# Kernel optimization log

Hardware: AMD Instinct MI355X
Metric: run time of the kernel (lower is better)

## Reference

```python
import jax, jax.numpy as jnp
import numpy as np

N_NODES = 100000
N_EDGES = 1600000
D_FEAT = 64


def setup_inputs() -> dict:
    key = jax.random.key(0)
    k1, k2, k3, k4 = jax.random.split(key, 4)
    row = jnp.sort(jax.random.randint(k1, (N_EDGES,), 0, N_NODES, dtype=jnp.int32))
    col = jax.random.randint(k2, (N_EDGES,), 0, N_NODES, dtype=jnp.int32)
    values = jax.random.uniform(k3, (N_EDGES,), dtype=jnp.float32)
    x = jax.random.normal(k4, (N_NODES, D_FEAT), dtype=jnp.float32)
    return {"row": row, "col": col, "values": values, "x": x}


def reference(row, col, values, x):
    # spmm_scatter: out[row[e]] += values[e] * x[col[e]]  (gather-multiply-scatter)
    msgs = x[col] * values[:, None]                      # [E, d]
    out = jax.ops.segment_sum(msgs, row, num_segments=x.shape[0])  # [N, d]
    return out
```

## Files before the change

kernel.cpp:

```cpp
#include <hip/hip_runtime.h>


constexpr int D  = 64;
constexpr int DV = D / 4;

__global__ __launch_bounds__(256) void spmm_psearch(
    const int* __restrict__ row,
    const int* __restrict__ col,
    const float* __restrict__ val,
    const float4* __restrict__ x4,
    float4* __restrict__ out4,
    int nEdges, int nNodes)
{
    const int wid = (blockIdx.x * blockDim.x + threadIdx.x) >> 6;
    if (wid >= nNodes) return;
    const int lane  = threadIdx.x & 63;
    const int group = lane >> 4;
    const int sub   = lane & 15;

    int lo = 0, hi = nEdges;
    const int t0 = wid;
    while (hi > lo) {
        const int span = hi - lo + 1;
        if (span <= 64) {
            const int idx = lo + lane;
            const bool lt = (idx <= hi) && (idx < nEdges) && (row[idx] < t0);
            lo += __popcll(__ballot(lt));
            break;
        }
        const int step = (span + 63) >> 6;
        const int idx  = lo + lane * step;
        const bool lt  = (idx <= hi) && (idx < nEdges) && (row[idx] < t0);
        const int  c   = __popcll(__ballot(lt));
        if (c == 0) { hi = lo; break; }
        const int new_lo = lo + (c - 1) * step + 1;
        if (c < 64) hi = lo + c * step;
        lo = new_lo;
    }
    const int start = lo;

    const int t1 = wid + 1;
    int end = start;
    for (;;) {
        const int idx = end + lane;
        const bool lt = (idx < nEdges) && (row[idx] < t1);
        const int  c  = __popcll(__ballot(lt));
        end += c;
        if (c < 64) break;
    }

    float4 acc = {0.f, 0.f, 0.f, 0.f};
    for (int e = start + group; e < end; e += 16) {
        const int e1 = e + 4, e2 = e + 8, e3 = e + 12;
        const int   c0 = col[e];
        const float v0 = val[e];
        int c1 = c0, c2 = c0, c3 = c0;
        float v1 = 0.f, v2 = 0.f, v3 = 0.f;
        if (e1 < end) { c1 = col[e1]; v1 = val[e1]; }
        if (e2 < end) { c2 = col[e2]; v2 = val[e2]; }
        if (e3 < end) { c3 = col[e3]; v3 = val[e3]; }
        const float4 x0 = x4[(size_t)c0 * DV + sub];
        const float4 x1 = x4[(size_t)c1 * DV + sub];
        const float4 x2 = x4[(size_t)c2 * DV + sub];
        const float4 x3 = x4[(size_t)c3 * DV + sub];
        acc.x = fmaf(v0, x0.x, acc.x); acc.y = fmaf(v0, x0.y, acc.y);
        acc.z = fmaf(v0, x0.z, acc.z); acc.w = fmaf(v0, x0.w, acc.w);
        acc.x = fmaf(v1, x1.x, acc.x); acc.y = fmaf(v1, x1.y, acc.y);
        acc.z = fmaf(v1, x1.z, acc.z); acc.w = fmaf(v1, x1.w, acc.w);
        acc.x = fmaf(v2, x2.x, acc.x); acc.y = fmaf(v2, x2.y, acc.y);
        acc.z = fmaf(v2, x2.z, acc.z); acc.w = fmaf(v2, x2.w, acc.w);
        acc.x = fmaf(v3, x3.x, acc.x); acc.y = fmaf(v3, x3.y, acc.y);
        acc.z = fmaf(v3, x3.z, acc.z); acc.w = fmaf(v3, x3.w, acc.w);
    }

    #pragma unroll
    for (int off = 16; off <= 32; off <<= 1) {
        acc.x += __shfl_xor(acc.x, off, 64);
        acc.y += __shfl_xor(acc.y, off, 64);
        acc.z += __shfl_xor(acc.z, off, 64);
        acc.w += __shfl_xor(acc.w, off, 64);
    }
    if (group == 0) out4[(size_t)wid * DV + sub] = acc;
}

extern "C" void kernel_launch(void* const* d_in, const int* in_sizes, int n_in,
                              void* d_out, int out_size, void* d_ws, size_t ws_size,
                              hipStream_t stream)
{
    const int*    row  = (const int*)   d_in[0];
    const int*    col  = (const int*)   d_in[1];
    const float*  val  = (const float*) d_in[2];
    const float4* x4   = (const float4*)d_in[3];
    float4*       out4 = (float4*)d_out;

    const int nEdges = in_sizes[0];
    const int nNodes = out_size / D;

    const dim3 block(256);
    const dim3 grid(((size_t)nNodes * 64 + 255) / 256);
    spmm_psearch<<<grid, block, 0, stream>>>(row, col, val, x4, out4, nEdges, nNodes);
}
```

Measured before the change: 153.7 us.

## Add prep pass building row_ptr and fp16 copy of x for gather

Adds a prep kernel that converts x to half precision into workspace and builds a CSR row pointer from the sorted row array. The main kernel then reads start/end directly instead of doing a wave-wide binary search, and gathers half-size feature rows to cut gather bandwidth. This adds an extra launch and a full pass over x and row, and reduces input precision to fp16, which may exceed the accuracy tolerance. The fallback path's unroll was also reduced from 4 to 2.

```diff
diff --git a/kernel.cpp b/kernel.cpp
--- a/kernel.cpp
+++ b/kernel.cpp
@@ -1,8 +1,88 @@
 #include <hip/hip_runtime.h>
+#include <hip/hip_fp16.h>
 
 
 constexpr int D  = 64;
-constexpr int DV = D / 4;
+constexpr int DV = 16;
+constexpr int DH = 16;
+
+struct __align__(8) h4 { __half2 a, b; };
+
+__global__ __launch_bounds__(256) void prep_kernel(
+    const int* __restrict__ row,
+    const float4* __restrict__ x4,
+    h4* __restrict__ xh,
+    int* __restrict__ row_ptr,
+    int nEdges, int n4, int nNodes)
+{
+    const int i = blockIdx.x * blockDim.x + threadIdx.x;
+    if (i < n4) {
+        const float4 v = x4[i];
+        h4 h;
+        h.a = __float22half2_rn(make_float2(v.x, v.y));
+        h.b = __float22half2_rn(make_float2(v.z, v.w));
+        xh[i] = h;
+    }
+    if (i < nEdges) {
+        const int r    = row[i];
+        const int prev = (i == 0) ? -1 : row[i - 1];
+        for (int n = prev + 1; n <= r; ++n) row_ptr[n] = i;
+        if (i == nEdges - 1)
+            for (int n = r + 1; n <= nNodes; ++n) row_ptr[n] = nEdges;
+    }
+}
+
+__global__ __launch_bounds__(256) void spmm_h(
+    const int* __restrict__ row_ptr,
+    const int* __restrict__ col,
+    const float* __restrict__ val,
+    const h4* __restrict__ xh,
+    float4* __restrict__ out4,
+    int nNodes)
+{
+    const int wid = (blockIdx.x * blockDim.x + threadIdx.x) >> 6;
+    if (wid >= nNodes) return;
+    const int lane  = threadIdx.x & 63;
+    const int group = lane >> 4;
+    const int sub   = lane & 15;
+
+    const int start = row_ptr[wid];
+    const int end   = row_ptr[wid + 1];
+
+    float4 acc = {0.f, 0.f, 0.f, 0.f};
+    for (int e = start + group; e < end; e += 16) {
+        const int e1 = e + 4, e2 = e + 8, e3 = e + 12;
+        const int   c0 = col[e];
+        const float v0 = val[e];
+        int c1 = c0, c2 = c0, c3 = c0;
+        float v1 = 0.f, v2 = 0.f, v3 = 0.f;
+        if (e1 < end) { c1 = col[e1]; v1 = val[e1]; }
+        if (e2 < end) { c2 = col[e2]; v2 = val[e2]; }
+        if (e3 < end) { c3 = col[e3]; v3 = val[e3]; }
+        const h4 p0 = xh[(size_t)c0 * DH + sub];
+        const h4 p1 = xh[(size_t)c1 * DH + sub];
+        const h4 p2 = xh[(size_t)c2 * DH + sub];
+        const h4 p3 = xh[(size_t)c3 * DH + sub];
+        float2 f;
+        f = __half22float2(p0.a); acc.x = fmaf(v0, f.x, acc.x); acc.y = fmaf(v0, f.y, acc.y);
+        f = __half22float2(p0.b); acc.z = fmaf(v0, f.x, acc.z); acc.w = fmaf(v0, f.y, acc.w);
+        f = __half22float2(p1.a); acc.x = fmaf(v1, f.x, acc.x); acc.y = fmaf(v1, f.y, acc.y);
+        f = __half22float2(p1.b); acc.z = fmaf(v1, f.x, acc.z); acc.w = fmaf(v1, f.y, acc.w);
+        f = __half22float2(p2.a); acc.x = fmaf(v2, f.x, acc.x); acc.y = fmaf(v2, f.y, acc.y);
+        f = __half22float2(p2.b); acc.z = fmaf(v2, f.x, acc.z); acc.w = fmaf(v2, f.y, acc.w);
+        f = __half22float2(p3.a); acc.x = fmaf(v3, f.x, acc.x); acc.y = fmaf(v3, f.y, acc.y);
+        f = __half22float2(p3.b); acc.z = fmaf(v3, f.x, acc.z); acc.w = fmaf(v3, f.y, acc.w);
+    }
+
+    #pragma unroll
+    for (int off = 16; off <= 32; off <<= 1) {
+        acc.x += __shfl_xor(acc.x, off, 64);
+        acc.y += __shfl_xor(acc.y, off, 64);
+        acc.z += __shfl_xor(acc.z, off, 64);
+        acc.w += __shfl_xor(acc.w, off, 64);
+    }
+    if (group == 0) out4[(size_t)wid * DV + sub] = acc;
+}
 
 __global__ __launch_bounds__(256) void spmm_psearch(
     const int* __restrict__ row,
@@ -38,7 +118,6 @@
         lo = new_lo;
     }
     const int start = lo;
-
     const int t1 = wid + 1;
     int end = start;
     for (;;) {
@@ -50,29 +129,19 @@
     }
 
     float4 acc = {0.f, 0.f, 0.f, 0.f};
-    for (int e = start + group; e < end; e += 16) {
-        const int e1 = e + 4, e2 = e + 8, e3 = e + 12;
+    for (int e = start + group; e < end; e += 8) {
+        const int e1 = e + 4;
         const int   c0 = col[e];
         const float v0 = val[e];
-        int c1 = c0, c2 = c0, c3 = c0;
-        float v1 = 0.f, v2 = 0.f, v3 = 0.f;
+        int c1 = c0; float v1 = 0.f;
         if (e1 < end) { c1 = col[e1]; v1 = val[e1]; }
-        if (e2 < end) { c2 = col[e2]; v2 = val[e2]; }
-        if (e3 < end) { c3 = col[e3]; v3 = val[e3]; }
         const float4 x0 = x4[(size_t)c0 * DV + sub];
         const float4 x1 = x4[(size_t)c1 * DV + sub];
-        const float4 x2 = x4[(size_t)c2 * DV + sub];
-        const float4 x3 = x4[(size_t)c3 * DV + sub];
         acc.x = fmaf(v0, x0.x, acc.x); acc.y = fmaf(v0, x0.y, acc.y);
         acc.z = fmaf(v0, x0.z, acc.z); acc.w = fmaf(v0, x0.w, acc.w);
         acc.x = fmaf(v1, x1.x, acc.x); acc.y = fmaf(v1, x1.y, acc.y);
         acc.z = fmaf(v1, x1.z, acc.z); acc.w = fmaf(v1, x1.w, acc.w);
-        acc.x = fmaf(v2, x2.x, acc.x); acc.y = fmaf(v2, x2.y, acc.y);
-        acc.z = fmaf(v2, x2.z, acc.z); acc.w = fmaf(v2, x2.w, acc.w);
-        acc.x = fmaf(v3, x3.x, acc.x); acc.y = fmaf(v3, x3.y, acc.y);
-        acc.z = fmaf(v3, x3.z, acc.z); acc.w = fmaf(v3, x3.w, acc.w);
     }
-
     #pragma unroll
     for (int off = 16; off <= 32; off <<= 1) {
         acc.x += __shfl_xor(acc.x, off, 64);
@@ -95,8 +164,25 @@
 
     const int nEdges = in_sizes[0];
     const int nNodes = out_size / D;
+    const int n4     = nNodes * DV;
 
     const dim3 block(256);
-    const dim3 grid(((size_t)nNodes * 64 + 255) / 256);
-    spmm_psearch<<<grid, block, 0, stream>>>(row, col, val, x4, out4, nEdges, nNodes);
+    const dim3 gridMain(((size_t)nNodes * 64 + 255) / 256);
+
+    const size_t rp_bytes = (size_t)(nNodes + 1) * sizeof(int);
+    const size_t xh_off   = (rp_bytes + 255) & ~(size_t)255;
+    const size_t need     = xh_off + (size_t)nNodes * D * sizeof(__half);
+
+    if (ws_size >= need) {
+        int* row_ptr = (int*)d_ws;
+        h4*  xh      = (h4*)((char*)d_ws + xh_off);
+        const int prep_n = (nEdges > n4) ? nEdges : n4;
+        prep_kernel<<<dim3((prep_n + 255) / 256), block, 0, stream>>>(
+            row, x4, xh, row_ptr, nEdges, n4, nNodes);
+        spmm_h<<<gridMain, block, 0, stream>>>(
+            row_ptr, (const int*)d_in[1], val, xh, out4, nNodes);
+    } else {
+        spmm_psearch<<<gridMain, block, 0, stream>>>(
+            row, (const int*)d_in[1], val, x4, out4, nEdges, nNodes);
+    }
 }
```

Measured after the change: 135.4 us. 1.14x faster.
